# Kernel tuning notes

Measured on AMD Instinct MI355X. Metric: run time of the kernel, lower is better.

## Reference

```python
import jax, jax.numpy as jnp
import numpy as np

EMBED_SIZE = 384
HEAD_SIZE = 64

def setup_inputs() -> dict:
    key = jax.random.key(0)
    kx, kk, kq, kv = jax.random.split(key, 4)
    B, T, C = 8, 4096, EMBED_SIZE
    scale = 1.0 / np.sqrt(C)  # torch Linear default init is U(-1/sqrt(in),1/sqrt(in)); use small gaussian
    x = jax.random.normal(kx, (B, T, C), dtype=jnp.float32)
    Wk = jax.random.normal(kk, (C, HEAD_SIZE), dtype=jnp.float32) * scale  # stored as [in,out]
    Wq = jax.random.normal(kq, (C, HEAD_SIZE), dtype=jnp.float32) * scale
    Wv = jax.random.normal(kv, (C, HEAD_SIZE), dtype=jnp.float32) * scale
    return {"x": x, "Wk": Wk, "Wq": Wq, "Wv": Wv}

def reference(x, Wk, Wq, Wv):
    B, T, C = x.shape
    k = jnp.einsum('btc,ch->bth', x, Wk)
    q = jnp.einsum('btc,ch->bth', x, Wq)
    v = jnp.einsum('btc,ch->bth', x, Wv)
    # NOTE: original scales by C**0.5 (embed size), not head_size**0.5
    wei = jnp.einsum('bth,bsh->bts', q, k) / jnp.sqrt(jnp.float32(C))  # [B,T,T]
    causal = jnp.tril(jnp.ones((T, T), dtype=bool))
    wei = jnp.where(causal, wei, -jnp.inf)
    wei = jax.nn.softmax(wei, axis=-1)
    # dropout omitted (eval/deterministic mode)
    out = jnp.einsum('bts,bsh->bth', wei, v)
    return out
```

## Files before the change

### kernel.cpp

```cpp
#include <hip/hip_runtime.h>
#include <hip/hip_bf16.h>
#include <math.h>

#define EMBED 384
#define HD 64

typedef unsigned short u16;
typedef unsigned int u32;
using bf16x8 = __attribute__((ext_vector_type(8))) __bf16;
using f32x16 = __attribute__((ext_vector_type(16))) float;

__device__ inline u16 f2bf(float f) {
    union { float f; unsigned u; } v; v.f = f;
    unsigned r = v.u + 0x7fffu + ((v.u >> 16) & 1u);
    return (u16)(r >> 16);
}
__device__ inline bf16x8 ld16(const u16* p) { return *(const bf16x8*)p; }
__device__ inline u32 cvtpk(float lo, float hi) {
    u32 r;
    asm("v_cvt_pk_bf16_f32 %0, %1, %2" : "=v"(r) : "v"(lo), "v"(hi));
    return r;
}

__global__ __launch_bounds__(256) void wconv(
    const float* __restrict__ Wk, const float* __restrict__ Wq,
    const float* __restrict__ Wv, u16* __restrict__ Wt)
{
    const int idx = blockIdx.x * 256 + threadIdx.x;
    if (idx >= 192 * EMBED) return;
    const int col = idx / EMBED, k = idx - col * EMBED;
    const int mat = col >> 6, c2 = col & 63;
    const float* W = (mat == 0) ? Wk : (mat == 1) ? Wq : Wv;
    float v = W[k * HD + c2];
    if (mat == 1) v *= 0.051031036307982884f * 1.4426950408889634f;
    Wt[idx] = f2bf(v);
}

#define PSTEP(kk, XA, XB, WCUR, WNXT)                                          \
  {                                                                            \
    union { u32 u[4]; bf16x8 v; } bf;                                          \
    bf.u[0] = cvtpk(XA.x, XA.y); bf.u[1] = cvtpk(XA.z, XA.w);                  \
    bf.u[2] = cvtpk(XB.x, XB.y); bf.u[3] = cvtpk(XB.z, XB.w);                  \
    if ((kk) + 1 < 24) {                                                       \
      _Pragma("unroll")                                                        \
      for (int g = 0; g < 6; ++g)                                              \
        WNXT[g] = ld16(wb + (size_t)g * 32 * EMBED + ((kk) + 1) * 16);         \
    }                                                                          \
    _Pragma("unroll")                                                          \
    for (int g = 0; g < 6; ++g)                                                \
      acc[g] = __builtin_amdgcn_mfma_f32_32x32x16_bf16(WCUR[g], bf.v, acc[g], 0, 0, 0); \
    if ((kk) + 4 < 24) {                                                       \
      XA = *(const float4*)(xr + ((kk) + 4) * 16);                             \
      XB = *(const float4*)(xr + ((kk) + 4) * 16 + 4);                         \
    }                                                                          \
  }

__global__ __launch_bounds__(64) void proj_mfma(
    const float* __restrict__ x, const u16* __restrict__ Wt,
    u16* __restrict__ kb, u16* __restrict__ qb, u16* __restrict__ vtb, int T)
{
    const int lane = threadIdx.x;
    const int c = lane & 31, h = lane >> 5;
    const int tok = blockIdx.x * 32 + c;
    const float* xr = x + (size_t)tok * EMBED + 8 * h;
    const u16* wb = Wt + (size_t)c * EMBED + 8 * h;

    f32x16 acc[6];
    #pragma unroll
    for (int g = 0; g < 6; ++g)
        #pragma unroll
        for (int r = 0; r < 16; ++r) acc[g][r] = 0.f;

    float4 x0a = *(const float4*)(xr);
    float4 x0b = *(const float4*)(xr + 4);
    float4 x1a = *(const float4*)(xr + 16);
    float4 x1b = *(const float4*)(xr + 20);
    float4 x2a = *(const float4*)(xr + 32);
    float4 x2b = *(const float4*)(xr + 36);
    float4 x3a = *(const float4*)(xr + 48);
    float4 x3b = *(const float4*)(xr + 52);

    bf16x8 wfA[6], wfB[6];
    #pragma unroll
    for (int g = 0; g < 6; ++g) wfA[g] = ld16(wb + (size_t)g * 32 * EMBED);

    for (int k4 = 0; k4 < 24; k4 += 4) {
        PSTEP(k4 + 0, x0a, x0b, wfA, wfB)
        PSTEP(k4 + 1, x1a, x1b, wfB, wfA)
        PSTEP(k4 + 2, x2a, x2b, wfA, wfB)
        PSTEP(k4 + 3, x3a, x3b, wfB, wfA)
    }

    #pragma unroll
    for (int mat = 0; mat < 2; ++mat) {
        u16* dst = (mat == 0) ? kb : qb;
        #pragma unroll
        for (int dg = 0; dg < 2; ++dg) {
            const f32x16 a = acc[mat * 2 + dg];
            #pragma unroll
            for (int k2 = 0; k2 < 4; ++k2) {
                u32 pair[2];
                pair[0] = cvtpk(a[4 * k2], a[4 * k2 + 1]);
                pair[1] = cvtpk(a[4 * k2 + 2], a[4 * k2 + 3]);
                *(uint2*)(dst + (size_t)tok * HD + dg * 32 + 8 * k2 + 4 * h) = *(uint2*)pair;
            }
        }
    }
    const int bb = tok / T, trow = tok - bb * T;
    u16* vb = vtb + (size_t)bb * HD * T + trow;
    #pragma unroll
    for (int dg = 0; dg < 2; ++dg) {
        const f32x16 a = acc[4 + dg];
        #pragma unroll
        for (int r = 0; r < 16; ++r) {
            const int dim = (r & 3) + 8 * (r >> 2) + 4 * h + 32 * dg;
            vb[(size_t)dim * T] = f2bf(a[r]);
        }
    }
}

__global__ __launch_bounds__(256) void attn_mfma(
    const u16* __restrict__ qb, const u16* __restrict__ kb,
    const u16* __restrict__ vtb, float* __restrict__ out, int T)
{
    __shared__ float slab[4][HD][32];
    __shared__ float ml2[2][4][32];
    __shared__ float linv_s[32];

    const int b    = blockIdx.x;
    const int q32  = gridDim.y - 1 - blockIdx.y;
    const int qs   = q32 * 32;
    const int wv   = threadIdx.x >> 6;
    const int lane = threadIdx.x & 63;
    const int c = lane & 31, h = lane >> 5;

    bf16x8 qf[4];
    const u16* qp = qb + ((size_t)b * T + qs + c) * HD + 8 * h;
    #pragma unroll
    for (int kk = 0; kk < 4; ++kk) qf[kk] = ld16(qp + kk * 16);

    f32x16 o0, o1;
    #pragma unroll
    for (int r = 0; r < 16; ++r) { o0[r] = 0.f; o1[r] = 0.f; }
    float m = -INFINITY, lsum = 0.f;

    const u16* kbase  = kb  + (size_t)b * T * HD;
    const u16* vtbase = vtb + (size_t)b * HD * T;

    for (int s = wv; s <= q32; s += 4) {
        const u16* kp = kbase + (size_t)(32 * s + c) * HD + 8 * h;
        bf16x8 kf0 = ld16(kp), kf1 = ld16(kp + 16), kf2 = ld16(kp + 32), kf3 = ld16(kp + 48);
        const u16* vp = vtbase + (size_t)c * T + 32 * s + 8 * h;
        const bf16x8 vf00 = ld16(vp), vf01 = ld16(vp + 16);
        const u16* vp2 = vp + (size_t)32 * T;
        const bf16x8 vf10 = ld16(vp2), vf11 = ld16(vp2 + 16);

        f32x16 st;
        #pragma unroll
        for (int r = 0; r < 16; ++r) st[r] = 0.f;
        st = __builtin_amdgcn_mfma_f32_32x32x16_bf16(kf0, qf[0], st, 0, 0, 0);
        st = __builtin_amdgcn_mfma_f32_32x32x16_bf16(kf1, qf[1], st, 0, 0, 0);
        st = __builtin_amdgcn_mfma_f32_32x32x16_bf16(kf2, qf[2], st, 0, 0, 0);
        st = __builtin_amdgcn_mfma_f32_32x32x16_bf16(kf3, qf[3], st, 0, 0, 0);

        if (s == q32) {
            #pragma unroll
            for (int r = 0; r < 16; ++r) {
                const int key = (r & 3) + 8 * (r >> 2) + 4 * h;
                if (key > c) st[r] = -INFINITY;
            }
        }
        float tm = st[0];
        #pragma unroll
        for (int r = 1; r < 16; ++r) tm = fmaxf(tm, st[r]);
        tm = fmaxf(tm, __shfl_xor(tm, 32));
        if (__any(tm > m + 11.5f)) {
            const float mn = fmaxf(m, tm);
            const float corr = exp2f(m - mn);
            m = mn;
            lsum *= corr;
            #pragma unroll
            for (int r = 0; r < 16; ++r) { o0[r] *= corr; o1[r] *= corr; }
        }
        float ps = 0.f;
        #pragma unroll
        for (int r = 0; r < 16; ++r) { st[r] = exp2f(st[r] - m); ps += st[r]; }
        lsum += ps + __shfl_xor(ps, 32);
        u32 w[8];
        #pragma unroll
        for (int q = 0; q < 8; ++q) w[q] = cvtpk(st[2 * q], st[2 * q + 1]);
        #pragma unroll
        for (int ks2 = 0; ks2 < 2; ++ks2) {
            const u32 x0 = __shfl_xor(w[4 * ks2 + 0], 32);
            const u32 x1 = __shfl_xor(w[4 * ks2 + 1], 32);
            const u32 x2 = __shfl_xor(w[4 * ks2 + 2], 32);
            const u32 x3 = __shfl_xor(w[4 * ks2 + 3], 32);
            union { u32 u[4]; bf16x8 v; } pf;
            if (h == 0) { pf.u[0] = w[4*ks2];   pf.u[1] = w[4*ks2+1]; pf.u[2] = x0; pf.u[3] = x1; }
            else        { pf.u[0] = x2;         pf.u[1] = x3;         pf.u[2] = w[4*ks2+2]; pf.u[3] = w[4*ks2+3]; }
            if (ks2 == 0) {
                o0 = __builtin_amdgcn_mfma_f32_32x32x16_bf16(vf00, pf.v, o0, 0, 0, 0);
                o1 = __builtin_amdgcn_mfma_f32_32x32x16_bf16(vf10, pf.v, o1, 0, 0, 0);
            } else {
                o0 = __builtin_amdgcn_mfma_f32_32x32x16_bf16(vf01, pf.v, o0, 0, 0, 0);
                o1 = __builtin_amdgcn_mfma_f32_32x32x16_bf16(vf11, pf.v, o1, 0, 0, 0);
            }
        }
    }

    if (h == 0) { ml2[0][wv][c] = m; ml2[1][wv][c] = lsum; }
    __syncthreads();
    float M = -INFINITY;
    #pragma unroll
    for (int i = 0; i < 4; ++i) M = fmaxf(M, ml2[0][i][c]);
    float L = 0.f;
    #pragma unroll
    for (int i = 0; i < 4; ++i) L += ml2[1][i][c] * exp2f(ml2[0][i][c] - M);
    const float coef = exp2f(m - M);
    if (wv == 0 && h == 0) linv_s[c] = 1.f / L;
    #pragma unroll
    for (int r = 0; r < 16; ++r) {
        const int d0 = (r & 3) + 8 * (r >> 2) + 4 * h;
        slab[wv][d0][c]      = o0[r] * coef;
        slab[wv][d0 + 32][c] = o1[r] * coef;
    }
    __syncthreads();

    float res[8];
    #pragma unroll
    for (int j = 0; j < 8; ++j) {
        const int d = 16 * wv + 8 * h + j;
        res[j] = slab[0][d][c] + slab[1][d][c] + slab[2][d][c] + slab[3][d][c];
    }
    const float li = linv_s[c];
    float4 s0 = {res[0] * li, res[1] * li, res[2] * li, res[3] * li};
    float4 s1 = {res[4] * li, res[5] * li, res[6] * li, res[7] * li};
    float* op = out + ((size_t)b * T + qs + c) * HD + 16 * wv + 8 * h;
    *(float4*)op = s0;
    *(float4*)(op + 4) = s1;
}

extern "C" void kernel_launch(void* const* d_in, const int* in_sizes, int n_in,
                              void* d_out, int out_size, void* d_ws, size_t ws_size,
                              hipStream_t stream) {
    const float* x  = (const float*)d_in[0];
    const float* Wk = (const float*)d_in[1];
    const float* Wq = (const float*)d_in[2];
    const float* Wv = (const float*)d_in[3];
    float* out = (float*)d_out;

    const int M = in_sizes[0] / EMBED;
    const int B = 8;
    const int T = M / B;

    u16* kb  = (u16*)d_ws;
    u16* qb  = kb + (size_t)M * HD;
    u16* vtb = qb + (size_t)M * HD;
    u16* Wt  = vtb + (size_t)M * HD;

    wconv<<<(192 * EMBED + 255) / 256, 256, 0, stream>>>(Wk, Wq, Wv, Wt);
    proj_mfma<<<M / 32, 64, 0, stream>>>(x, Wt, kb, qb, vtb, T);
    dim3 g(B, T / 32);
    attn_mfma<<<g, 256, 0, stream>>>(qb, kb, vtb, out, T);
}
```

Before: 184.1 us.

## Double-buffer K loads, use permlane32 swap, and raise MFMA priority

Restructures the attention loop so the K tile for the next iteration is loaded into a second register set while the current tile is computed, hiding global load latency. Replaces the four cross-half shuffles used to rebuild the P fragment with v_permlane32_swap instructions. Wraps MFMA groups in s_setprio to favour matrix issue across waves. Costs extra VGPRs for the second K buffer, which may reduce occupancy.

```diff
diff --git a/kernel.cpp b/kernel.cpp
--- a/kernel.cpp
+++ b/kernel.cpp
@@ -20,6 +20,9 @@
     u32 r;
     asm("v_cvt_pk_bf16_f32 %0, %1, %2" : "=v"(r) : "v"(lo), "v"(hi));
     return r;
+}
+__device__ inline void plswap(u32& a, u32& b) {
+    asm volatile("v_permlane32_swap_b32 %0, %1" : "+v"(a), "+v"(b));
 }
 
 __global__ __launch_bounds__(256) void wconv(
@@ -119,6 +122,72 @@
     }
 }
 
+#define LOADK(KF0, KF1, KF2, KF3, S)                                            \
+  { const u16* kp_ = kbase + (size_t)(32 * (S) + c) * HD + 8 * h;               \
+    KF0 = ld16(kp_); KF1 = ld16(kp_ + 16); KF2 = ld16(kp_ + 32); KF3 = ld16(kp_ + 48); }
+
+#define COMPUTE(KF0, KF1, KF2, KF3, S)                                          \
+  { const u16* vp_ = vtbase + (size_t)c * T + 32 * (S) + 8 * h;                 \
+    const bf16x8 vf00 = ld16(vp_), vf01 = ld16(vp_ + 16);                       \
+    const u16* vp2_ = vp_ + (size_t)32 * T;                                     \
+    const bf16x8 vf10 = ld16(vp2_), vf11 = ld16(vp2_ + 16);                     \
+    f32x16 st;                                                                  \
+    _Pragma("unroll")                                                           \
+    for (int r = 0; r < 16; ++r) st[r] = 0.f;                                   \
+    __builtin_amdgcn_s_setprio(1);                                              \
+    st = __builtin_amdgcn_mfma_f32_32x32x16_bf16(KF0, qf0, st, 0, 0, 0);        \
+    st = __builtin_amdgcn_mfma_f32_32x32x16_bf16(KF1, qf1, st, 0, 0, 0);        \
+    st = __builtin_amdgcn_mfma_f32_32x32x16_bf16(KF2, qf2, st, 0, 0, 0);        \
+    st = __builtin_amdgcn_mfma_f32_32x32x16_bf16(KF3, qf3, st, 0, 0, 0);        \
+    __builtin_amdgcn_s_setprio(0);                                              \
+    if ((S) == q32) {                                                           \
+      _Pragma("unroll")                                                         \
+      for (int r = 0; r < 16; ++r) {                                            \
+        const int key = (r & 3) + 8 * (r >> 2) + 4 * h;                         \
+        if (key > c) st[r] = -INFINITY;                                         \
+      }                                                                         \
+    }                                                                           \
+    float tm = fmaxf(st[0], st[1]);                                             \
+    _Pragma("unroll")                                                           \
+    for (int r = 2; r < 16; ++r) tm = fmaxf(tm, st[r]);                         \
+    tm = fmaxf(tm, __shfl_xor(tm, 32));                                         \
+    if (__any(tm > m + 11.5f)) {                                                \
+      const float mn = fmaxf(m, tm);                                            \
+      const float corr = exp2f(m - mn);                                         \
+      m = mn;                                                                   \
+      lsum *= corr;                                                             \
+      _Pragma("unroll")                                                         \
+      for (int r = 0; r < 16; ++r) { o0[r] *= corr; o1[r] *= corr; }            \
+    }                                                                           \
+    float ps = 0.f;                                                             \
+    _Pragma("unroll")                                                           \
+    for (int r = 0; r < 16; ++r) { st[r] = exp2f(st[r] - m); ps += st[r]; }     \
+    lsum += ps + __shfl_xor(ps, 32);                                            \
+    u32 w[8];                                                                   \
+    _Pragma("unroll")                                                           \
+    for (int q = 0; q < 8; ++q) w[q] = cvtpk(st[2 * q], st[2 * q + 1]);         \
+    {                                                                           \
+      u32 a0 = w[0], b0 = w[2], a1 = w[1], b1 = w[3];                           \
+      plswap(a0, b0); plswap(a1, b1);                                           \
+      union { u32 u[4]; bf16x8 v; } pf;                                         \
+      pf.u[0] = a0; pf.u[1] = a1; pf.u[2] = b0; pf.u[3] = b1;                   \
+      __builtin_amdgcn_s_setprio(1);                                            \
+      o0 = __builtin_amdgcn_mfma_f32_32x32x16_bf16(vf00, pf.v, o0, 0, 0, 0);    \
+      o1 = __builtin_amdgcn_mfma_f32_32x32x16_bf16(vf10, pf.v, o1, 0, 0, 0);    \
+      __builtin_amdgcn_s_setprio(0);                                            \
+    }                                                                           \
+    {                                                                           \
+      u32 a0 = w[4], b0 = w[6], a1 = w[5], b1 = w[7];                           \
+      plswap(a0, b0); plswap(a1, b1);                                           \
+      union { u32 u[4]; bf16x8 v; } pf;                                         \
+      pf.u[0] = a0; pf.u[1] = a1; pf.u[2] = b0; pf.u[3] = b1;                   \
+      __builtin_amdgcn_s_setprio(1);                                            \
+      o0 = __builtin_amdgcn_mfma_f32_32x32x16_bf16(vf01, pf.v, o0, 0, 0, 0);    \
+      o1 = __builtin_amdgcn_mfma_f32_32x32x16_bf16(vf11, pf.v, o1, 0, 0, 0);    \
+      __builtin_amdgcn_s_setprio(0);                                            \
+    }                                                                           \
+  }
+
 __global__ __launch_bounds__(256) void attn_mfma(
     const u16* __restrict__ qb, const u16* __restrict__ kb,
     const u16* __restrict__ vtb, float* __restrict__ out, int T)
@@ -134,10 +203,9 @@
     const int lane = threadIdx.x & 63;
     const int c = lane & 31, h = lane >> 5;
 
-    bf16x8 qf[4];
     const u16* qp = qb + ((size_t)b * T + qs + c) * HD + 8 * h;
-    #pragma unroll
-    for (int kk = 0; kk < 4; ++kk) qf[kk] = ld16(qp + kk * 16);
+    const bf16x8 qf0 = ld16(qp), qf1 = ld16(qp + 16);
+    const bf16x8 qf2 = ld16(qp + 32), qf3 = ld16(qp + 48);
 
     f32x16 o0, o1;
     #pragma unroll
@@ -147,64 +215,22 @@
     const u16* kbase  = kb  + (size_t)b * T * HD;
     const u16* vtbase = vtb + (size_t)b * HD * T;
 
-    for (int s = wv; s <= q32; s += 4) {
-        const u16* kp = kbase + (size_t)(32 * s + c) * HD + 8 * h;
-        bf16x8 kf0 = ld16(kp), kf1 = ld16(kp + 16), kf2 = ld16(kp + 32), kf3 = ld16(kp + 48);
-        const u16* vp = vtbase + (size_t)c * T + 32 * s + 8 * h;
-        const bf16x8 vf00 = ld16(vp), vf01 = ld16(vp + 16);
-        const u16* vp2 = vp + (size_t)32 * T;
-        const bf16x8 vf10 = ld16(vp2), vf11 = ld16(vp2 + 16);
-
-        f32x16 st;
-        #pragma unroll
-        for (int r = 0; r < 16; ++r) st[r] = 0.f;
-        st = __builtin_amdgcn_mfma_f32_32x32x16_bf16(kf0, qf[0], st, 0, 0, 0);
-        st = __builtin_amdgcn_mfma_f32_32x32x16_bf16(kf1, qf[1], st, 0, 0, 0);
-        st = __builtin_amdgcn_mfma_f32_32x32x16_bf16(kf2, qf[2], st, 0, 0, 0);
-        st = __builtin_amdgcn_mfma_f32_32x32x16_bf16(kf3, qf[3], st, 0, 0, 0);
-
-        if (s == q32) {
-            #pragma unroll
-            for (int r = 0; r < 16; ++r) {
-                const int key = (r & 3) + 8 * (r >> 2) + 4 * h;
-                if (key > c) st[r] = -INFINITY;
-            }
-        }
-        float tm = st[0];
-        #pragma unroll
-        for (int r = 1; r < 16; ++r) tm = fmaxf(tm, st[r]);
-        tm = fmaxf(tm, __shfl_xor(tm, 32));
-        if (__any(tm > m + 11.5f)) {
-            const float mn = fmaxf(m, tm);
-            const float corr = exp2f(m - mn);
-            m = mn;
-            lsum *= corr;
-            #pragma unroll
-            for (int r = 0; r < 16; ++r) { o0[r] *= corr; o1[r] *= corr; }
-        }
-        float ps = 0.f;
-        #pragma unroll
-        for (int r = 0; r < 16; ++r) { st[r] = exp2f(st[r] - m); ps += st[r]; }
-        lsum += ps + __shfl_xor(ps, 32);
-        u32 w[8];
-        #pragma unroll
-        for (int q = 0; q < 8; ++q) w[q] = cvtpk(st[2 * q], st[2 * q + 1]);
-        #pragma unroll
-        for (int ks2 = 0; ks2 < 2; ++ks2) {
-            const u32 x0 = __shfl_xor(w[4 * ks2 + 0], 32);
-            const u32 x1 = __shfl_xor(w[4 * ks2 + 1], 32);
-            const u32 x2 = __shfl_xor(w[4 * ks2 + 2], 32);
-            const u32 x3 = __shfl_xor(w[4 * ks2 + 3], 32);
-            union { u32 u[4]; bf16x8 v; } pf;
-            if (h == 0) { pf.u[0] = w[4*ks2];   pf.u[1] = w[4*ks2+1]; pf.u[2] = x0; pf.u[3] = x1; }
-            else        { pf.u[0] = x2;         pf.u[1] = x3;         pf.u[2] = w[4*ks2+2]; pf.u[3] = w[4*ks2+3]; }
-            if (ks2 == 0) {
-                o0 = __builtin_amdgcn_mfma_f32_32x32x16_bf16(vf00, pf.v, o0, 0, 0, 0);
-                o1 = __builtin_amdgcn_mfma_f32_32x32x16_bf16(vf10, pf.v, o1, 0, 0, 0);
-            } else {
-                o0 = __builtin_amdgcn_mfma_f32_32x32x16_bf16(vf01, pf.v, o0, 0, 0, 0);
-                o1 = __builtin_amdgcn_mfma_f32_32x32x16_bf16(vf11, pf.v, o1, 0, 0, 0);
-            }
+    bf16x8 kA0, kA1, kA2, kA3, kB0, kB1, kB2, kB3;
+    int s = wv;
+    if (s <= q32) {
+        LOADK(kA0, kA1, kA2, kA3, s)
+        for (;;) {
+            const int sn = s + 4;
+            const bool hn = sn <= q32;
+            if (hn) { LOADK(kB0, kB1, kB2, kB3, sn) }
+            COMPUTE(kA0, kA1, kA2, kA3, s)
+            if (!hn) break;
+            const int sn2 = sn + 4;
+            const bool hn2 = sn2 <= q32;
+            if (hn2) { LOADK(kA0, kA1, kA2, kA3, sn2) }
+            COMPUTE(kB0, kB1, kB2, kB3, sn)
+            if (!hn2) break;
+            s = sn2;
         }
     }
 
```

New measurement: 184.9 us. About the same (+0.4%).
